# Optimization experiments

Hardware: AMD Instinct MI355X
Metric: run time of the kernel (lower is better)

Reference implementation:

```python
import jax, jax.numpy as jnp
import numpy as np

IN_FEATURES = 4096
OUT_FEATURES = 4096
ALPHA = 0.01  # dequant scale = input_scale * weight_scale
BETA = 1.0


def setup_inputs() -> dict:
    key = jax.random.key(0)
    kx, kw, kb = jax.random.split(key, 3)
    # int8 activations (W8A8): values in [-127, 127]
    x = jax.random.randint(kx, (4, 2048, IN_FEATURES), -127, 128, dtype=jnp.int8)
    # int8 weight buffer, [out_features, in_features] as in the torch module
    weight = jax.random.randint(kw, (OUT_FEATURES, IN_FEATURES), -127, 128, dtype=jnp.int8)
    # fp32 bias, [1, out_features]
    bias = jax.random.normal(kb, (1, OUT_FEATURES), dtype=jnp.float32)
    alpha = jnp.float32(ALPHA)
    return {"x": x, "weight": weight, "bias": bias, "alpha": alpha}


def reference(x, weight, bias, alpha):
    # y = alpha * (x_int8 @ W_int8^T) + beta * bias, accumulated in int32, output fp32
    x_shape = x.shape
    x2 = x.reshape(-1, x_shape[-1])  # [B*S, in]
    # int8 GEMM with int32 accumulation (faithful to the fused kernel's math)
    acc = jax.lax.dot_general(
        x2, weight,
        dimension_numbers=(((1,), (1,)), ((), ())),
        preferred_element_type=jnp.int32,
    )  # [B*S, out]
    y = alpha * acc.astype(jnp.float32) + BETA * bias  # fused dequant + bias
    return y.reshape(*x_shape[:-1], OUT_FEATURES)
```

## Files before the change

### kernel.cpp

```cpp
#include <hip/hip_runtime.h>
#include <stdint.h>

typedef int v4i __attribute__((ext_vector_type(4)));

constexpr int K_DIM = 4096;
constexpr int N_DIM = 4096;
constexpr int TM = 128;
constexpr int TN = 128;
constexpr int TK = 128;
constexpr int KSTEPS = K_DIM / TK;

__device__ __forceinline__ int pack4(int a, int b, int c, int d) {
    unsigned r = (unsigned(a) & 0xFFu)
               | ((unsigned(b) & 0xFFu) << 8)
               | ((unsigned(c) & 0xFFu) << 16)
               | (unsigned(d) << 24);
    return (int)r;
}

__global__ __launch_bounds__(256) void pack_both(
    const int* __restrict__ s1, int* __restrict__ d1, int n1,
    const int* __restrict__ s2, int* __restrict__ d2, int n2)
{
    int idx = blockIdx.x * blockDim.x + threadIdx.x;
    const int* s;
    int* d;
    if (idx < n1) { s = s1; d = d1; }
    else if (idx < n1 + n2) { s = s2; d = d2; idx -= n1; }
    else return;
    v4i v = ((const v4i*)s)[idx];
    d[idx] = pack4(v.x, v.y, v.z, v.w);
}

__device__ __forceinline__ void gld16(const int8_t* g, int8_t* l) {
    __builtin_amdgcn_global_load_lds(
        (const __attribute__((address_space(1))) char*)g,
        (__attribute__((address_space(3))) char*)l,
        16, 0, 0);
}

constexpr int BM = 256;
constexpr int BN = 256;
constexpr int BKB = 128;
constexpr int KT = K_DIM / BKB;

__global__ __launch_bounds__(512, 2) void w8a8_gemm_256(
    const int8_t* __restrict__ X,
    const int8_t* __restrict__ Wt,
    const float*  __restrict__ bias,
    const float*  __restrict__ alphap,
    float* __restrict__ Y)
{
    extern __shared__ __align__(128) int8_t smem[];

    const int tid  = threadIdx.x;
    const int lane = tid & 63;
    const int wave = tid >> 6;

    const int flat = blockIdx.x;
    const int swz  = (flat & 7) * 64 + (flat >> 3);
    const int m0   = (swz & 31) * BM;
    const int n0   = (swz >> 5) * BN;

    int ag[4], bg[4], ldso[4];
#pragma unroll
    for (int q = 0; q < 4; ++q) {
        const int c   = q * 512 + tid;
        const int row = c >> 3;
        const int gko = ((c & 7) ^ ((row >> 1) & 7)) << 4;
        ag[q]   = (m0 + row) * K_DIM + gko;
        bg[q]   = (n0 + row) * K_DIM + gko;
        ldso[q] = c << 4;
    }

    const int wm   = (wave & 1) << 7;
    const int wn   = (wave >> 1) << 6;
    const int lrow = lane & 15;
    const int quad = lane >> 4;

    int a_off[8], b_off[4];
#pragma unroll
    for (int i = 0; i < 8; ++i) {
        const int ra = wm + i * 16 + lrow;
        a_off[i] = ra * BKB + ((quad ^ ((ra >> 1) & 7)) << 4);
    }
#pragma unroll
    for (int j = 0; j < 4; ++j) {
        const int rb = wn + j * 16 + lrow;
        b_off[j] = rb * BKB + ((quad ^ ((rb >> 1) & 7)) << 4);
    }

    v4i acc[8][4] = {};

#pragma unroll
    for (int q = 0; q < 4; ++q) gld16(X  + ag[q], smem + ldso[q]);
#pragma unroll
    for (int q = 0; q < 4; ++q) gld16(Wt + bg[q], smem + 32768 + ldso[q]);

    for (int t = 0; t < KT; ++t) {
        int8_t* Ard = smem + ((t & 1) << 16);
        int8_t* Brd = Ard + 32768;
        const int kb1 = (t + 1) * BKB;

        if (t + 1 < KT) {
            int8_t* Awr = smem + (((t + 1) & 1) << 16);
#pragma unroll
            for (int q = 0; q < 4; ++q) gld16(X + ag[q] + kb1, Awr + ldso[q]);
            asm volatile("s_waitcnt vmcnt(4)" ::: "memory");
        } else {
            asm volatile("s_waitcnt vmcnt(0)" ::: "memory");
        }
        asm volatile("s_barrier" ::: "memory");

        v4i a[8], b[4];
#pragma unroll
        for (int i = 0; i < 8; ++i) a[i] = *(const v4i*)(Ard + a_off[i]);
#pragma unroll
        for (int j = 0; j < 4; ++j) b[j] = *(const v4i*)(Brd + b_off[j]);
        __builtin_amdgcn_s_setprio(1);
#pragma unroll
        for (int i = 0; i < 8; ++i)
#pragma unroll
            for (int j = 0; j < 4; ++j)
                acc[i][j] = __builtin_amdgcn_mfma_i32_16x16x64_i8(a[i], b[j], acc[i][j], 0, 0, 0);
        __builtin_amdgcn_s_setprio(0);

        if (t + 1 < KT) {
            int8_t* Bwr = smem + (((t + 1) & 1) << 16) + 32768;
#pragma unroll
            for (int q = 0; q < 4; ++q) gld16(Wt + bg[q] + kb1, Bwr + ldso[q]);
        }

#pragma unroll
        for (int i = 0; i < 8; ++i) a[i] = *(const v4i*)(Ard + (a_off[i] ^ 64));
#pragma unroll
        for (int j = 0; j < 4; ++j) b[j] = *(const v4i*)(Brd + (b_off[j] ^ 64));
        __builtin_amdgcn_s_setprio(1);
#pragma unroll
        for (int i = 0; i < 8; ++i)
#pragma unroll
            for (int j = 0; j < 4; ++j)
                acc[i][j] = __builtin_amdgcn_mfma_i32_16x16x64_i8(a[i], b[j], acc[i][j], 0, 0, 0);
        __builtin_amdgcn_s_setprio(0);

        asm volatile("s_barrier" ::: "memory");
    }

    const float alpha = *alphap;
#pragma unroll
    for (int j = 0; j < 4; ++j) {
        const int col = n0 + wn + j * 16 + lrow;
        const float bj = bias[col];
#pragma unroll
        for (int i = 0; i < 8; ++i) {
            const size_t rbase = (size_t)(m0 + wm + i * 16 + quad * 4) * N_DIM + col;
#pragma unroll
            for (int r = 0; r < 4; ++r)
                Y[rbase + (size_t)r * N_DIM] = fmaf(alpha, (float)acc[i][j][r], bj);
        }
    }
}

__global__ __launch_bounds__(256) void w8a8_gemm_packed(
    const int8_t* __restrict__ X,
    const int8_t* __restrict__ Wt,
    const float*  __restrict__ bias,
    const float*  __restrict__ alphap,
    float* __restrict__ Y)
{
    __shared__ __align__(16) int8_t As[TM * TK];
    __shared__ __align__(16) int8_t Bs[TN * TK];

    const int tid  = threadIdx.x;
    const int lane = tid & 63;
    const int wave = tid >> 6;

    const int m0 = blockIdx.x * TM;
    const int n0 = blockIdx.y * TN;

    const int8_t* Aga[4];
    const int8_t* Bga[4];
    int lds_off[4];
#pragma unroll
    for (int i = 0; i < 4; ++i) {
        const int c    = (wave * 4 + i) * 64 + lane;
        const int row  = c >> 3;
        const int gko  = ((c & 7) ^ ((row >> 1) & 7)) << 4;
        Aga[i] = X  + (size_t)(m0 + row) * K_DIM + gko;
        Bga[i] = Wt + (size_t)(n0 + row) * K_DIM + gko;
        lds_off[i] = c << 4;
    }

    const int wm   = (wave & 1) << 6;
    const int wn   = (wave >> 1) << 6;
    const int lrow = lane & 15;
    const int quad = lane >> 4;

    int a_off[4], b_off[4];
#pragma unroll
    for (int i = 0; i < 4; ++i) {
        const int ra = wm + i * 16 + lrow;
        a_off[i] = ra * TK + ((quad ^ ((ra >> 1) & 7)) << 4);
        const int rb = wn + i * 16 + lrow;
        b_off[i] = rb * TK + ((quad ^ ((rb >> 1) & 7)) << 4);
    }

    v4i acc[4][4] = {};

    for (int kt = 0; kt < KSTEPS; ++kt) {
        const int kb = kt * TK;
#pragma unroll
        for (int i = 0; i < 4; ++i) {
            gld16(Aga[i] + kb, As + lds_off[i]);
            gld16(Bga[i] + kb, Bs + lds_off[i]);
        }
        __syncthreads();

#pragma unroll
        for (int kk = 0; kk < 2; ++kk) {
            const int kx = kk << 6;
            v4i a[4], b[4];
#pragma unroll
            for (int i = 0; i < 4; ++i) a[i] = *(const v4i*)(As + (a_off[i] ^ kx));
#pragma unroll
            for (int j = 0; j < 4; ++j) b[j] = *(const v4i*)(Bs + (b_off[j] ^ kx));
#pragma unroll
            for (int i = 0; i < 4; ++i)
#pragma unroll
                for (int j = 0; j < 4; ++j)
                    acc[i][j] = __builtin_amdgcn_mfma_i32_16x16x64_i8(a[i], b[j], acc[i][j], 0, 0, 0);
        }

        __syncthreads();
    }

    const float alpha = *alphap;
#pragma unroll
    for (int j = 0; j < 4; ++j) {
        const int col = n0 + wn + j * 16 + lrow;
        const float bj = bias[col];
#pragma unroll
        for (int i = 0; i < 4; ++i) {
            const size_t rbase = (size_t)(m0 + wm + i * 16 + quad * 4) * N_DIM + col;
#pragma unroll
            for (int r = 0; r < 4; ++r)
                Y[rbase + (size_t)r * N_DIM] = fmaf(alpha, (float)acc[i][j][r], bj);
        }
    }
}

__global__ __launch_bounds__(256, 2) void w8a8_gemm_fb(
    const int*   __restrict__ X,
    const int*   __restrict__ Wt,
    const float* __restrict__ bias,
    const float* __restrict__ alphap,
    float* __restrict__ Y)
{
    __shared__ __align__(16) int8_t As[TM * 64];
    __shared__ __align__(16) int8_t Bs[TN * 64];

    const int tid  = threadIdx.x;
    const int lane = tid & 63;
    const int wave = tid >> 6;
    const int m0 = blockIdx.x * TM;
    const int n0 = blockIdx.y * TN;

    const int srow = tid >> 3;
    const int sk   = (tid & 7) * 8;
    const int* Ag = X  + (size_t)(m0 + srow) * K_DIM + sk;
    const int* Bg = Wt + (size_t)(n0 + srow) * K_DIM + sk;

    int wr_off[4];
#pragma unroll
    for (int r = 0; r < 4; ++r) {
        const int row = r * 32 + (tid >> 3);
        const int dw  = (tid & 7) * 2;
        const int sw  = row * 16 + (((dw >> 2) ^ ((row >> 1) & 3)) << 2) + (dw & 3);
        wr_off[r] = sw * 4;
    }

    const int wm   = (wave & 1) << 6;
    const int wn   = (wave >> 1) << 6;
    const int lrow = lane & 15;
    const int quad = lane >> 4;

    int a_off[4], b_off[4];
#pragma unroll
    for (int i = 0; i < 4; ++i) {
        const int ra = wm + i * 16 + lrow;
        a_off[i] = ra * 64 + ((quad ^ ((ra >> 1) & 3)) << 4);
        const int rb = wn + i * 16 + lrow;
        b_off[i] = rb * 64 + ((quad ^ ((rb >> 1) & 3)) << 4);
    }

    v4i acc[4][4] = {};
    v4i av[8], bv[8];
#pragma unroll
    for (int r = 0; r < 4; ++r) {
        const int* pa = Ag + (size_t)r * 32 * K_DIM;
        const int* pb = Bg + (size_t)r * 32 * K_DIM;
        av[2 * r] = *(const v4i*)(pa);  av[2 * r + 1] = *(const v4i*)(pa + 4);
        bv[2 * r] = *(const v4i*)(pb);  bv[2 * r + 1] = *(const v4i*)(pb + 4);
    }

    for (int kt = 0; kt < 64; ++kt) {
#pragma unroll
        for (int r = 0; r < 4; ++r) {
            int2 pa2, pb2;
            pa2.x = pack4(av[2*r].x,   av[2*r].y,   av[2*r].z,   av[2*r].w);
            pa2.y = pack4(av[2*r+1].x, av[2*r+1].y, av[2*r+1].z, av[2*r+1].w);
            pb2.x = pack4(bv[2*r].x,   bv[2*r].y,   bv[2*r].z,   bv[2*r].w);
            pb2.y = pack4(bv[2*r+1].x, bv[2*r+1].y, bv[2*r+1].z, bv[2*r+1].w);
            *(int2*)(As + wr_off[r]) = pa2;
            *(int2*)(Bs + wr_off[r]) = pb2;
        }
        const int kn = (kt + 1 < 64) ? (kt + 1) : kt;
        const int koff = kn * 64;
#pragma unroll
        for (int r = 0; r < 4; ++r) {
            const int* pa = Ag + (size_t)r * 32 * K_DIM + koff;
            const int* pb = Bg + (size_t)r * 32 * K_DIM + koff;
            av[2 * r] = *(const v4i*)(pa);  av[2 * r + 1] = *(const v4i*)(pa + 4);
            bv[2 * r] = *(const v4i*)(pb);  bv[2 * r + 1] = *(const v4i*)(pb + 4);
        }
        __syncthreads();
        v4i a[4], b[4];
#pragma unroll
        for (int i = 0; i < 4; ++i) a[i] = *(const v4i*)(As + a_off[i]);
#pragma unroll
        for (int j = 0; j < 4; ++j) b[j] = *(const v4i*)(Bs + b_off[j]);
#pragma unroll
        for (int i = 0; i < 4; ++i)
#pragma unroll
            for (int j = 0; j < 4; ++j)
                acc[i][j] = __builtin_amdgcn_mfma_i32_16x16x64_i8(a[i], b[j], acc[i][j], 0, 0, 0);
        __syncthreads();
    }

    const float alpha = *alphap;
#pragma unroll
    for (int j = 0; j < 4; ++j) {
        const int col = n0 + wn + j * 16 + lrow;
        const float bj = bias[col];
#pragma unroll
        for (int i = 0; i < 4; ++i) {
            const size_t rbase = (size_t)(m0 + wm + i * 16 + quad * 4) * N_DIM + col;
#pragma unroll
            for (int r = 0; r < 4; ++r)
                Y[rbase + (size_t)r * N_DIM] = fmaf(alpha, (float)acc[i][j][r], bj);
        }
    }
}

extern "C" void kernel_launch(void* const* d_in, const int* in_sizes, int n_in,
                              void* d_out, int out_size, void* d_ws, size_t ws_size,
                              hipStream_t stream) {
    const int*   X32   = (const int*)d_in[0];
    const int*   W32   = (const int*)d_in[1];
    const float* bias  = (const float*)d_in[2];
    const float* alpha = (const float*)d_in[3];
    float* Y = (float*)d_out;

    const int nX = in_sizes[0];
    const int nW = in_sizes[1];
    const int M  = nX / K_DIM;

    if (ws_size >= (size_t)nX + (size_t)nW) {
        int8_t* Xp = (int8_t*)d_ws;
        int8_t* Wp = Xp + nX;
        const int n1 = nX / 4, n2 = nW / 4;
        const int nthreads = n1 + n2;
        pack_both<<<(nthreads + 255) / 256, 256, 0, stream>>>(
            X32, (int*)Xp, n1, W32, (int*)Wp, n2);

        static hipError_t attr = hipFuncSetAttribute(
            reinterpret_cast<const void*>(w8a8_gemm_256),
            hipFuncAttributeMaxDynamicSharedMemorySize, 131072);

        if (attr == hipSuccess && (M % BM) == 0) {
            const int nblocks = (M / BM) * (N_DIM / BN);
            w8a8_gemm_256<<<dim3(nblocks), dim3(512), 131072, stream>>>(
                Xp, Wp, bias, alpha, Y);
        } else {
            dim3 grid(M / TM, N_DIM / TN);
            w8a8_gemm_packed<<<grid, dim3(256), 0, stream>>>(Xp, Wp, bias, alpha, Y);
        }
    } else {
        dim3 grid(M / TM, N_DIM / TN);
        w8a8_gemm_fb<<<grid, dim3(256), 0, stream>>>(X32, W32, bias, alpha, Y);
    }
}
```

Before: 391.6 us.

## Switch GEMM mainloop to 4-stage K=64 pipeline with one barrier per step

```diff
diff --git a/kernel.cpp b/kernel.cpp
--- a/kernel.cpp
+++ b/kernel.cpp
@@ -41,10 +41,10 @@
 
 constexpr int BM = 256;
 constexpr int BN = 256;
-constexpr int BKB = 128;
-constexpr int KT = K_DIM / BKB;
-
-__global__ __launch_bounds__(512, 2) void w8a8_gemm_256(
+constexpr int HKB = 64;
+constexpr int NH = K_DIM / HKB;
+
+__global__ __launch_bounds__(512, 2) void w8a8_gemm_256p(
     const int8_t* __restrict__ X,
     const int8_t* __restrict__ Wt,
     const float*  __restrict__ bias,
@@ -62,15 +62,15 @@
     const int m0   = (swz & 31) * BM;
     const int n0   = (swz >> 5) * BN;
 
-    int ag[4], bg[4], ldso[4];
-#pragma unroll
-    for (int q = 0; q < 4; ++q) {
+    int ga[2], gb[2], ls[2];
+#pragma unroll
+    for (int q = 0; q < 2; ++q) {
         const int c   = q * 512 + tid;
-        const int row = c >> 3;
-        const int gko = ((c & 7) ^ ((row >> 1) & 7)) << 4;
-        ag[q]   = (m0 + row) * K_DIM + gko;
-        bg[q]   = (n0 + row) * K_DIM + gko;
-        ldso[q] = c << 4;
+        const int row = c >> 2;
+        const int sl  = ((c & 3) ^ ((row >> 1) & 3)) << 4;
+        ga[q] = (m0 + row) * K_DIM + sl;
+        gb[q] = (n0 + row) * K_DIM + sl;
+        ls[q] = c << 4;
     }
 
     const int wm   = (wave & 1) << 7;
@@ -82,69 +82,74 @@
 #pragma unroll
     for (int i = 0; i < 8; ++i) {
         const int ra = wm + i * 16 + lrow;
-        a_off[i] = ra * BKB + ((quad ^ ((ra >> 1) & 7)) << 4);
+        a_off[i] = ra * HKB + ((quad ^ ((ra >> 1) & 3)) << 4);
     }
 #pragma unroll
     for (int j = 0; j < 4; ++j) {
         const int rb = wn + j * 16 + lrow;
-        b_off[j] = rb * BKB + ((quad ^ ((rb >> 1) & 7)) << 4);
+        b_off[j] = 16384 + rb * HKB + ((quad ^ ((rb >> 1) & 3)) << 4);
     }
 
     v4i acc[8][4] = {};
 
 #pragma unroll
-    for (int q = 0; q < 4; ++q) gld16(X  + ag[q], smem + ldso[q]);
-#pragma unroll
-    for (int q = 0; q < 4; ++q) gld16(Wt + bg[q], smem + 32768 + ldso[q]);
-
-    for (int t = 0; t < KT; ++t) {
-        int8_t* Ard = smem + ((t & 1) << 16);
-        int8_t* Brd = Ard + 32768;
-        const int kb1 = (t + 1) * BKB;
-
-        if (t + 1 < KT) {
-            int8_t* Awr = smem + (((t + 1) & 1) << 16);
-#pragma unroll
-            for (int q = 0; q < 4; ++q) gld16(X + ag[q] + kb1, Awr + ldso[q]);
-            asm volatile("s_waitcnt vmcnt(4)" ::: "memory");
-        } else {
-            asm volatile("s_waitcnt vmcnt(0)" ::: "memory");
-        }
-        asm volatile("s_barrier" ::: "memory");
-
-        v4i a[8], b[4];
-#pragma unroll
-        for (int i = 0; i < 8; ++i) a[i] = *(const v4i*)(Ard + a_off[i]);
-#pragma unroll
-        for (int j = 0; j < 4; ++j) b[j] = *(const v4i*)(Brd + b_off[j]);
-        __builtin_amdgcn_s_setprio(1);
-#pragma unroll
-        for (int i = 0; i < 8; ++i)
-#pragma unroll
-            for (int j = 0; j < 4; ++j)
-                acc[i][j] = __builtin_amdgcn_mfma_i32_16x16x64_i8(a[i], b[j], acc[i][j], 0, 0, 0);
-        __builtin_amdgcn_s_setprio(0);
-
-        if (t + 1 < KT) {
-            int8_t* Bwr = smem + (((t + 1) & 1) << 16) + 32768;
-#pragma unroll
-            for (int q = 0; q < 4; ++q) gld16(Wt + bg[q] + kb1, Bwr + ldso[q]);
-        }
-
-#pragma unroll
-        for (int i = 0; i < 8; ++i) a[i] = *(const v4i*)(Ard + (a_off[i] ^ 64));
-#pragma unroll
-        for (int j = 0; j < 4; ++j) b[j] = *(const v4i*)(Brd + (b_off[j] ^ 64));
-        __builtin_amdgcn_s_setprio(1);
-#pragma unroll
-        for (int i = 0; i < 8; ++i)
-#pragma unroll
-            for (int j = 0; j < 4; ++j)
-                acc[i][j] = __builtin_amdgcn_mfma_i32_16x16x64_i8(a[i], b[j], acc[i][j], 0, 0, 0);
-        __builtin_amdgcn_s_setprio(0);
-
-        asm volatile("s_barrier" ::: "memory");
-    }
+    for (int p = 0; p < 3; ++p) {
+        int8_t* ib = smem + (p << 15);
+        const int kb = p * HKB;
+        gld16(X  + ga[0] + kb, ib + ls[0]);
+        gld16(X  + ga[1] + kb, ib + ls[1]);
+        gld16(Wt + gb[0] + kb, ib + 16384 + ls[0]);
+        gld16(Wt + gb[1] + kb, ib + 16384 + ls[1]);
+    }
+
+#define KHALF_BODY(VMN, DOISS)                                               \
+    {                                                                        \
+        asm volatile("s_waitcnt vmcnt(" #VMN ")" ::: "memory");              \
+        __builtin_amdgcn_s_barrier();                                        \
+        int8_t* Ab = smem + ((h & 3) << 15);                                 \
+        if (DOISS) {                                                         \
+            int8_t* ib  = smem + (((h + 3) & 3) << 15);                      \
+            const int k3 = (h + 3) * HKB;                                    \
+            gld16(X + ga[0] + k3, ib + ls[0]);                               \
+            gld16(X + ga[1] + k3, ib + ls[1]);                               \
+        }                                                                    \
+        v4i a[8], b[4];                                                      \
+        _Pragma("unroll")                                                    \
+        for (int i = 0; i < 4; ++i) a[i] = *(const v4i*)(Ab + a_off[i]);     \
+        _Pragma("unroll")                                                    \
+        for (int j = 0; j < 4; ++j) b[j] = *(const v4i*)(Ab + b_off[j]);     \
+        __builtin_amdgcn_s_setprio(1);                                       \
+        _Pragma("unroll")                                                    \
+        for (int i = 0; i < 4; ++i)                                          \
+            _Pragma("unroll")                                                \
+            for (int j = 0; j < 4; ++j)                                      \
+                acc[i][j] = __builtin_amdgcn_mfma_i32_16x16x64_i8(           \
+                    a[i], b[j], acc[i][j], 0, 0, 0);                         \
+        __builtin_amdgcn_s_setprio(0);                                       \
+        if (DOISS) {                                                         \
+            int8_t* ib  = smem + (((h + 3) & 3) << 15);                      \
+            const int k3 = (h + 3) * HKB;                                    \
+            gld16(Wt + gb[0] + k3, ib + 16384 + ls[0]);                      \
+            gld16(Wt + gb[1] + k3, ib + 16384 + ls[1]);                      \
+        }                                                                    \
+        _Pragma("unroll")                                                    \
+        for (int i = 4; i < 8; ++i) a[i] = *(const v4i*)(Ab + a_off[i]);     \
+        __builtin_amdgcn_s_setprio(1);                                       \
+        _Pragma("unroll")                                                    \
+        for (int i = 4; i < 8; ++i)                                          \
+            _Pragma("unroll")                                                \
+            for (int j = 0; j < 4; ++j)                                      \
+                acc[i][j] = __builtin_amdgcn_mfma_i32_16x16x64_i8(           \
+                    a[i], b[j], acc[i][j], 0, 0, 0);                         \
+        __builtin_amdgcn_s_setprio(0);                                       \
+    }
+
+#pragma unroll 1
+    for (int h = 0; h < 61; ++h) KHALF_BODY(8, true)
+    { const int h = 61; KHALF_BODY(8, false) }
+    { const int h = 62; KHALF_BODY(4, false) }
+    { const int h = 63; KHALF_BODY(0, false) }
+#undef KHALF_BODY
 
     const float alpha = *alphap;
 #pragma unroll
@@ -374,12 +379,12 @@
             X32, (int*)Xp, n1, W32, (int*)Wp, n2);
 
         static hipError_t attr = hipFuncSetAttribute(
-            reinterpret_cast<const void*>(w8a8_gemm_256),
+            reinterpret_cast<const void*>(w8a8_gemm_256p),
             hipFuncAttributeMaxDynamicSharedMemorySize, 131072);
 
         if (attr == hipSuccess && (M % BM) == 0) {
             const int nblocks = (M / BM) * (N_DIM / BN);
-            w8a8_gemm_256<<<dim3(nblocks), dim3(512), 131072, stream>>>(
+            w8a8_gemm_256p<<<dim3(nblocks), dim3(512), 131072, stream>>>(
                 Xp, Wp, bias, alpha, Y);
         } else {
             dim3 grid(M / TM, N_DIM / TN);
```

Measured after the change: 388.5 us. About the same (-0.8%).
